# Optimization experiments

Measured on AMD Instinct MI355X. Metric: run time of the kernel, lower is better.

Reference implementation:

```python
import jax, jax.numpy as jnp
import numpy as np

B, T, I, H, O = 64, 1024, 256, 512, 128


def setup_inputs() -> dict:
    key = jax.random.key(0)
    ks = jax.random.split(key, 12)
    s = 1.0 / np.sqrt(H)  # PyTorch LSTM init: U(-1/sqrt(H), 1/sqrt(H))
    u = lambda k, shape: jax.random.uniform(k, shape, jnp.float32, -s, s)
    return {
        "inputs": jax.random.normal(ks[0], (B, T, I), jnp.float32),
        "W_ih_f": u(ks[1], (4 * H, I)),
        "W_hh_f": u(ks[2], (4 * H, H)),
        "b_ih_f": u(ks[3], (4 * H,)),
        "b_hh_f": u(ks[4], (4 * H,)),
        "W_ih_b": u(ks[5], (4 * H, I)),
        "W_hh_b": u(ks[6], (4 * H, H)),
        "b_ih_b": u(ks[7], (4 * H,)),
        "b_hh_b": u(ks[8], (4 * H,)),
        "W_out": u(ks[9], (O, 2 * H)),
        "b_out": u(ks[10], (O,)),
    }


def _lstm_dir(inputs, W_ih, W_hh, b_ih, b_hh, reverse):
    # Precompute input contribution for all timesteps: [B,T,4H] -> [T,B,4H]
    xg = jnp.einsum("bti,gi->btg", inputs, W_ih) + b_ih + b_hh
    xg = jnp.swapaxes(xg, 0, 1)
    b = inputs.shape[0]
    h0 = jnp.zeros((b, H), inputs.dtype)
    c0 = jnp.zeros((b, H), inputs.dtype)

    def step(carry, x_t):
        h, c = carry
        gates = x_t + h @ W_hh.T  # [B,4H], PyTorch gate order i,f,g,o
        i, f, g, o = jnp.split(gates, 4, axis=-1)
        i = jax.nn.sigmoid(i)
        f = jax.nn.sigmoid(f)
        g = jnp.tanh(g)
        o = jax.nn.sigmoid(o)
        c = f * c + i * g
        h = o * jnp.tanh(c)
        return (h, c), h

    (hT, cT), hs = jax.lax.scan(step, (h0, c0), xg, reverse=reverse)
    return jnp.swapaxes(hs, 0, 1), hT, cT  # hs: [B,T,H]


def reference(inputs, W_ih_f, W_hh_f, b_ih_f, b_hh_f,
              W_ih_b, W_hh_b, b_ih_b, b_hh_b, W_out, b_out):
    y_f, h_f, c_f = _lstm_dir(inputs, W_ih_f, W_hh_f, b_ih_f, b_hh_f, False)
    y_b, h_b, c_b = _lstm_dir(inputs, W_ih_b, W_hh_b, b_ih_b, b_hh_b, True)
    y = jnp.concatenate([y_f, y_b], axis=-1)            # [B,T,2H]
    out = jnp.einsum("bth,oh->bto", y, W_out) + b_out    # [B,T,O]
    h_n = jnp.stack([h_f, h_b])                          # [2,B,H]
    c_n = jnp.stack([c_f, c_b])                          # [2,B,H]
    return out, h_n, c_n
```

## Files before the change

kernel.cpp:

```cpp
#include <hip/hip_runtime.h>
#include <stdint.h>

#define T_LEN 1024
#define B_SZ  64
#define I_SZ  256
#define H_SZ  512
#define O_SZ  128
#define WP    776

#define L1_OFF  0ull
#define HB_OFF  524288ull
#define Y_OFF   786432ull
#define XBF_OFF 135004160ull
#define MEMSET_BYTES 786432ull

typedef __attribute__((ext_vector_type(8))) short short8;
typedef __attribute__((ext_vector_type(4))) float f32x4;

__device__ __forceinline__ unsigned short f2bf(float f) {
  unsigned u = __float_as_uint(f);
  u += 0x7fffu + ((u >> 16) & 1u);
  return (unsigned short)(u >> 16);
}
__device__ __forceinline__ ushort4 cvt4(float4 v) {
  ushort4 p;
  p.x = f2bf(v.x); p.y = f2bf(v.y); p.z = f2bf(v.z); p.w = f2bf(v.w);
  return p;
}
__device__ __forceinline__ float sigm(float x) { return 1.0f / (1.0f + __expf(-x)); }
__device__ __forceinline__ float tanh_f(float x) { return 1.0f - 2.0f / (1.0f + __expf(2.0f * x)); }

__global__ void __launch_bounds__(256) cvt_x(const float* __restrict__ x,
                                             unsigned short* __restrict__ xb) {
  size_t i = ((size_t)blockIdx.x * 256 + threadIdx.x) * 8;
  float4 a = *(const float4*)(x + i);
  float4 b = *(const float4*)(x + i + 4);
  *(ushort4*)(xb + i)     = cvt4(a);
  *(ushort4*)(xb + i + 4) = cvt4(b);
}

__global__ void __launch_bounds__(512, 2)
lstm_scan(const unsigned short* __restrict__ xbf,
          const float* __restrict__ WihF, const float* __restrict__ WhhF,
          const float* __restrict__ bihF, const float* __restrict__ bhhF,
          const float* __restrict__ WihB, const float* __restrict__ WhhB,
          const float* __restrict__ bihB, const float* __restrict__ bhhB,
          unsigned char* __restrict__ ws, float* __restrict__ out)
{
  __shared__ unsigned short xh[32 * WP];
  __shared__ float gbuf[4][32][18];
  __shared__ float cst[32][18];

  const int tid  = threadIdx.x;
  const int wave = tid >> 6;
  const int lane = tid & 63;
  const int nl   = lane & 15;
  const int q16  = lane >> 4;

  const int wg  = blockIdx.x;
  const int d   = wg >> 6;
  const int loc = wg & 63;
  const int b0  = (loc >> 5) * 32;
  const int u0  = (loc & 31) * 16;
  const int grp = wg >> 5;

  const float* Wih = d ? WihB : WihF;
  const float* Whh = d ? WhhB : WhhF;
  const float* bih = d ? bihB : bihF;
  const float* bhh = d ? bhhB : bhhF;

  const int gate = wave >> 1;
  const int mt   = wave & 1;

  short8 wfrag[24];
  {
    const int row = gate * H_SZ + u0 + nl;
    const float* wi = Wih + (size_t)row * I_SZ;
    const float* wh = Whh + (size_t)row * H_SZ;
#pragma unroll
    for (int kk = 0; kk < 24; ++kk) {
      const float* src = (kk < 8) ? (wi + kk * 32 + q16 * 8)
                                  : (wh + (kk - 8) * 32 + q16 * 8);
      float4 v0 = ((const float4*)src)[0];
      float4 v1 = ((const float4*)src)[1];
      short8 w;
      w[0] = (short)f2bf(v0.x); w[1] = (short)f2bf(v0.y);
      w[2] = (short)f2bf(v0.z); w[3] = (short)f2bf(v0.w);
      w[4] = (short)f2bf(v1.x); w[5] = (short)f2bf(v1.y);
      w[6] = (short)f2bf(v1.z); w[7] = (short)f2bf(v1.w);
      wfrag[kk] = w;
    }
  }
  const float bias = bih[gate * H_SZ + u0 + nl] + bhh[gate * H_SZ + u0 + nl];

  cst[tid >> 4][tid & 15] = 0.0f;

  unsigned* cntbase = (unsigned*)(ws + L1_OFF);
  unsigned* hbuf32  = (unsigned*)(ws + HB_OFF);
  unsigned* ybuf32  = (unsigned*)(ws + Y_OFF);
  unsigned* xh32    = (unsigned*)xh;

  const int sm = tid >> 4, sseg = tid & 15;

  int t_next = d ? (T_LEN - 1) : 0;
  uint4 px0, px1;
  {
    const uint4* src = (const uint4*)(xbf + ((size_t)(b0 + sm) * T_LEN + t_next) * I_SZ + sseg * 16);
    px0 = src[0]; px1 = src[1];
  }

  for (int s = 0; s < T_LEN; ++s) {
    const int t  = t_next;
    const int rb = (s & 1) ^ 1, wb = s & 1;

    {
      uint4* dst = (uint4*)(xh + sm * WP + sseg * 16);
      dst[0] = px0; dst[1] = px1;
    }
    {
      unsigned hv[16];
#pragma unroll
      for (int j = 0; j < 16; ++j) {
        int lin = j * 512 + tid;
        hv[j] = __hip_atomic_load(hbuf32 + ((size_t)((rb * 2 + d) * B_SZ + b0) * 256 + lin),
                                  __ATOMIC_RELAXED, __HIP_MEMORY_SCOPE_AGENT);
      }
#pragma unroll
      for (int j = 0; j < 16; ++j) {
        int lin = j * 512 + tid;
        int m = lin >> 8, col = lin & 255;
        xh32[m * (WP / 2) + 128 + col] = hv[j];
      }
    }
    __syncthreads();

    f32x4 acc = {0.f, 0.f, 0.f, 0.f};
    const unsigned short* ar = xh + (mt * 16 + nl) * WP + q16 * 8;
#pragma unroll
    for (int kk = 0; kk < 24; ++kk) {
      short8 a = *(const short8*)(ar + kk * 32);
      acc = __builtin_amdgcn_mfma_f32_16x16x32_bf16(a, wfrag[kk], acc, 0, 0, 0);
    }

#pragma unroll
    for (int r = 0; r < 4; ++r) {
      float v = acc[r] + bias;
      v = (gate == 2) ? tanh_f(v) : sigm(v);
      gbuf[gate][mt * 16 + q16 * 4 + r][nl] = v;
    }
    __syncthreads();

    {
      int m = tid >> 4, n = tid & 15;
      float gi = gbuf[0][m][n], gf = gbuf[1][m][n];
      float gg = gbuf[2][m][n], go = gbuf[3][m][n];
      float c = gf * cst[m][n] + gi * gg;
      cst[m][n] = c;
      float h = go * tanh_f(c);
      unsigned hbits = f2bf(h);
      unsigned other = __shfl_xor(hbits, 1);
      if ((tid & 1) == 0) {
        unsigned packed = hbits | (other << 16);
        size_t hi = (size_t)((wb * 2 + d) * B_SZ + b0 + m) * 256 + (u0 + n) / 2;
        __hip_atomic_store(hbuf32 + hi, packed, __ATOMIC_RELAXED, __HIP_MEMORY_SCOPE_AGENT);
        size_t yi = ((size_t)(b0 + m) * T_LEN + t) * 512 + (d * H_SZ + u0 + n) / 2;
        ybuf32[yi] = packed;
      }
      if (s == T_LEN - 1) {
        size_t hi = (size_t)(d * B_SZ + b0 + m) * H_SZ + u0 + n;
        out[8388608ull + hi] = h;
        out[8388608ull + 65536ull + hi] = c;
      }
    }

    if (s < T_LEN - 1) {
      t_next = d ? (T_LEN - 2 - s) : (s + 1);
      {
        const uint4* src = (const uint4*)(xbf + ((size_t)(b0 + sm) * T_LEN + t_next) * I_SZ + sseg * 16);
        px0 = src[0]; px1 = src[1];
      }
      __builtin_amdgcn_s_waitcnt(0);
      __syncthreads();
      if (tid == 0) {
        unsigned* cnt = cntbase + ((size_t)s * 4 + grp) * 32;
        __hip_atomic_fetch_add(cnt, 1u, __ATOMIC_RELAXED, __HIP_MEMORY_SCOPE_AGENT);
        while (__hip_atomic_load(cnt, __ATOMIC_RELAXED, __HIP_MEMORY_SCOPE_AGENT) < 32u)
          __builtin_amdgcn_s_sleep(1);
      }
      __syncthreads();
      __asm__ volatile("" ::: "memory");
    }
  }
}

__global__ void __launch_bounds__(256, 1)
proj(const unsigned short* __restrict__ y, const float* __restrict__ Wout,
     const float* __restrict__ bout, float* __restrict__ out)
{
  __shared__ unsigned short ys[128 * 264];
  __shared__ unsigned short wst[128 * 264];

  const int tid  = threadIdx.x;
  const int wave = tid >> 6;
  const int lane = tid & 63;
  const int nl   = lane & 15;
  const int q16  = lane >> 4;
  const int m0   = blockIdx.x * 128;

  f32x4 acc[2][8];
#pragma unroll
  for (int a = 0; a < 2; ++a)
#pragma unroll
    for (int b = 0; b < 8; ++b) acc[a][b] = (f32x4){0.f, 0.f, 0.f, 0.f};

  for (int k0 = 0; k0 < 1024; k0 += 256) {
    {
      int r = tid >> 1, half = tid & 1;
      const uint4* src = (const uint4*)(y + (size_t)(m0 + r) * 1024 + k0 + half * 128);
      uint4* dst = (uint4*)(ys + r * 264 + half * 128);
#pragma unroll
      for (int q = 0; q < 16; ++q) dst[q] = src[q];
    }
    {
      int r = tid >> 1, half = tid & 1;
      const float4* src = (const float4*)(Wout + (size_t)r * 1024 + k0 + half * 128);
      unsigned short* wd = wst + r * 264 + half * 128;
#pragma unroll
      for (int q = 0; q < 32; ++q) *(ushort4*)(wd + q * 4) = cvt4(src[q]);
    }
    __syncthreads();

#pragma unroll
    for (int kk = 0; kk < 8; ++kk) {
      const int ko = kk * 32 + q16 * 8;
      short8 bfr[8];
#pragma unroll
      for (int nt = 0; nt < 8; ++nt)
        bfr[nt] = *(const short8*)(wst + (nt * 16 + nl) * 264 + ko);
#pragma unroll
      for (int mtt = 0; mtt < 2; ++mtt) {
        short8 a = *(const short8*)(ys + ((wave * 2 + mtt) * 16 + nl) * 264 + ko);
#pragma unroll
        for (int nt = 0; nt < 8; ++nt)
          acc[mtt][nt] = __builtin_amdgcn_mfma_f32_16x16x32_bf16(a, bfr[nt], acc[mtt][nt], 0, 0, 0);
      }
    }
    __syncthreads();
  }

#pragma unroll
  for (int mtt = 0; mtt < 2; ++mtt) {
#pragma unroll
    for (int nt = 0; nt < 8; ++nt) {
      int col = nt * 16 + nl;
      float bo = bout[col];
      int rowb = m0 + (wave * 2 + mtt) * 16 + q16 * 4;
#pragma unroll
      for (int r = 0; r < 4; ++r)
        out[(size_t)(rowb + r) * O_SZ + col] = acc[mtt][nt][r] + bo;
    }
  }
}

extern "C" void kernel_launch(void* const* d_in, const int* in_sizes, int n_in,
                              void* d_out, int out_size, void* d_ws, size_t ws_size,
                              hipStream_t stream) {
  const float* x    = (const float*)d_in[0];
  const float* WihF = (const float*)d_in[1];
  const float* WhhF = (const float*)d_in[2];
  const float* bihF = (const float*)d_in[3];
  const float* bhhF = (const float*)d_in[4];
  const float* WihB = (const float*)d_in[5];
  const float* WhhB = (const float*)d_in[6];
  const float* bihB = (const float*)d_in[7];
  const float* bhhB = (const float*)d_in[8];
  const float* Wout = (const float*)d_in[9];
  const float* bout = (const float*)d_in[10];
  float* out = (float*)d_out;
  unsigned char* ws = (unsigned char*)d_ws;

  hipMemsetAsync(ws, 0, (size_t)MEMSET_BYTES, stream);
  cvt_x<<<8192, 256, 0, stream>>>(x, (unsigned short*)(ws + XBF_OFF));
  lstm_scan<<<128, 512, 0, stream>>>((const unsigned short*)(ws + XBF_OFF),
                                     WihF, WhhF, bihF, bhhF,
                                     WihB, WhhB, bihB, bhhB,
                                     ws, out);
  proj<<<512, 256, 0, stream>>>((const unsigned short*)(ws + Y_OFF), Wout, bout, out);
}
```

Measured before the change: 3.711 ms.

## Replace counter barrier with per-WG step flags and overlap x-projection with sync wait

Swaps the per-step atomic counter barrier (fetch_add plus a single-thread spin and two syncthreads) for per-workgroup monotonic step flags. A whole wave polls the flags and checks them with __all, so there is no atomic RMW and no sleep. The input-projection MFMAs for the next timestep are computed right after the flag is published, before waiting on other workgroups, which takes them off the serial critical path. The recurrent MFMA chain is split into two accumulators to shorten the dependency chain. In exchange, the x tile is double-buffered in LDS and the design depends on relaxed-ordering visibility of the h buffer across workgroups.

```diff
diff --git a/kernel.cpp b/kernel.cpp
--- a/kernel.cpp
+++ b/kernel.cpp
@@ -6,9 +6,8 @@
 #define I_SZ  256
 #define H_SZ  512
 #define O_SZ  128
-#define WP    776
-
-#define L1_OFF  0ull
+
+#define FLAG_OFF 0ull
 #define HB_OFF  524288ull
 #define Y_OFF   786432ull
 #define XBF_OFF 135004160ull
@@ -47,22 +46,24 @@
           const float* __restrict__ bihB, const float* __restrict__ bhhB,
           unsigned char* __restrict__ ws, float* __restrict__ out)
 {
-  __shared__ unsigned short xh[32 * WP];
+  __shared__ unsigned short xs[2][32][264];
+  __shared__ unsigned short hs[32][520];
   __shared__ float gbuf[4][32][18];
   __shared__ float cst[32][18];
 
   const int tid  = threadIdx.x;
+  const int lane = tid & 63;
   const int wave = tid >> 6;
-  const int lane = tid & 63;
   const int nl   = lane & 15;
   const int q16  = lane >> 4;
 
-  const int wg  = blockIdx.x;
-  const int d   = wg >> 6;
-  const int loc = wg & 63;
-  const int b0  = (loc >> 5) * 32;
-  const int u0  = (loc & 31) * 16;
-  const int grp = wg >> 5;
+  const int wg   = blockIdx.x;
+  const int d    = wg >> 6;
+  const int loc  = wg & 63;
+  const int b0   = (loc >> 5) * 32;
+  const int u0   = (loc & 31) * 16;
+  const int grp  = wg >> 5;
+  const int wgid = loc & 31;
 
   const float* Wih = d ? WihB : WihF;
   const float* Whh = d ? WhhB : WhhF;
@@ -95,56 +96,83 @@
 
   cst[tid >> 4][tid & 15] = 0.0f;
 
-  unsigned* cntbase = (unsigned*)(ws + L1_OFF);
-  unsigned* hbuf32  = (unsigned*)(ws + HB_OFF);
-  unsigned* ybuf32  = (unsigned*)(ws + Y_OFF);
-  unsigned* xh32    = (unsigned*)xh;
+  unsigned* flags  = (unsigned*)(ws + FLAG_OFF);
+  unsigned* hbuf32 = (unsigned*)(ws + HB_OFF);
+  unsigned* ybuf32 = (unsigned*)(ws + Y_OFF);
+  unsigned* hs32   = (unsigned*)hs;
 
   const int sm = tid >> 4, sseg = tid & 15;
 
-  int t_next = d ? (T_LEN - 1) : 0;
+  {
+    const int t0 = d ? (T_LEN - 1) : 0;
+    const uint4* src = (const uint4*)(xbf + ((size_t)(b0 + sm) * T_LEN + t0) * I_SZ + sseg * 16);
+    uint4 a = src[0], b = src[1];
+    uint4* dst = (uint4*)(&xs[0][sm][sseg * 16]);
+    dst[0] = a; dst[1] = b;
+  }
+  __syncthreads();
+  f32x4 xacc = {0.f, 0.f, 0.f, 0.f};
+  {
+    const unsigned short* xr = &xs[0][mt * 16 + nl][q16 * 8];
+#pragma unroll
+    for (int kk = 0; kk < 8; ++kk) {
+      short8 a = *(const short8*)(xr + kk * 32);
+      xacc = __builtin_amdgcn_mfma_f32_16x16x32_bf16(a, wfrag[kk], xacc, 0, 0, 0);
+    }
+  }
   uint4 px0, px1;
   {
-    const uint4* src = (const uint4*)(xbf + ((size_t)(b0 + sm) * T_LEN + t_next) * I_SZ + sseg * 16);
+    const int t1 = d ? (T_LEN - 2) : 1;
+    const uint4* src = (const uint4*)(xbf + ((size_t)(b0 + sm) * T_LEN + t1) * I_SZ + sseg * 16);
     px0 = src[0]; px1 = src[1];
   }
 
   for (int s = 0; s < T_LEN; ++s) {
-    const int t  = t_next;
-    const int rb = (s & 1) ^ 1, wb = s & 1;
-
-    {
-      uint4* dst = (uint4*)(xh + sm * WP + sseg * 16);
-      dst[0] = px0; dst[1] = px1;
-    }
+    const int t   = d ? (T_LEN - 1 - s) : s;
+    const int cur = s & 1, nxt = cur ^ 1;
+    const int rb  = cur ^ 1, wb = cur;
+
+    if (s > 0) {
+      const unsigned tgt = (unsigned)s;
+      unsigned* fl = flags + grp * 32;
+      for (;;) {
+        unsigned f = (lane < 32)
+          ? __hip_atomic_load(fl + lane, __ATOMIC_RELAXED, __HIP_MEMORY_SCOPE_AGENT)
+          : tgt;
+        if (__all((int)(f >= tgt))) break;
+      }
+    }
+
     {
       unsigned hv[16];
+      unsigned* hb = hbuf32 + (size_t)((rb * 2 + d) * B_SZ + b0) * 256;
+#pragma unroll
+      for (int j = 0; j < 16; ++j)
+        hv[j] = __hip_atomic_load(hb + j * 512 + tid, __ATOMIC_RELAXED, __HIP_MEMORY_SCOPE_AGENT);
 #pragma unroll
       for (int j = 0; j < 16; ++j) {
         int lin = j * 512 + tid;
-        hv[j] = __hip_atomic_load(hbuf32 + ((size_t)((rb * 2 + d) * B_SZ + b0) * 256 + lin),
-                                  __ATOMIC_RELAXED, __HIP_MEMORY_SCOPE_AGENT);
-      }
-#pragma unroll
-      for (int j = 0; j < 16; ++j) {
-        int lin = j * 512 + tid;
-        int m = lin >> 8, col = lin & 255;
-        xh32[m * (WP / 2) + 128 + col] = hv[j];
-      }
-    }
-    __syncthreads();
-
-    f32x4 acc = {0.f, 0.f, 0.f, 0.f};
-    const unsigned short* ar = xh + (mt * 16 + nl) * WP + q16 * 8;
-#pragma unroll
-    for (int kk = 0; kk < 24; ++kk) {
-      short8 a = *(const short8*)(ar + kk * 32);
-      acc = __builtin_amdgcn_mfma_f32_16x16x32_bf16(a, wfrag[kk], acc, 0, 0, 0);
+        hs32[(lin >> 8) * 260 + (lin & 255)] = hv[j];
+      }
+    }
+    __syncthreads();
+
+    f32x4 acc0 = xacc, acc1 = {0.f, 0.f, 0.f, 0.f};
+    {
+      const unsigned short* ar = &hs[mt * 16 + nl][q16 * 8];
+#pragma unroll
+      for (int kk = 0; kk < 16; kk += 2) {
+        short8 a0 = *(const short8*)(ar + kk * 32);
+        short8 a1 = *(const short8*)(ar + (kk + 1) * 32);
+        acc0 = __builtin_amdgcn_mfma_f32_16x16x32_bf16(a0, wfrag[8 + kk], acc0, 0, 0, 0);
+        acc1 = __builtin_amdgcn_mfma_f32_16x16x32_bf16(a1, wfrag[9 + kk], acc1, 0, 0, 0);
+      }
+      acc0 += acc1;
     }
 
 #pragma unroll
     for (int r = 0; r < 4; ++r) {
-      float v = acc[r] + bias;
+      float v = acc0[r] + bias;
       v = (gate == 2) ? tanh_f(v) : sigm(v);
       gbuf[gate][mt * 16 + q16 * 4 + r][nl] = v;
     }
@@ -174,21 +202,29 @@
     }
 
     if (s < T_LEN - 1) {
-      t_next = d ? (T_LEN - 2 - s) : (s + 1);
-      {
-        const uint4* src = (const uint4*)(xbf + ((size_t)(b0 + sm) * T_LEN + t_next) * I_SZ + sseg * 16);
+      uint4* dst = (uint4*)(&xs[nxt][sm][sseg * 16]);
+      dst[0] = px0; dst[1] = px1;
+    }
+    __builtin_amdgcn_s_waitcnt(0);
+    __syncthreads();
+
+    if (s < T_LEN - 1) {
+      if (tid == 0)
+        __hip_atomic_store(flags + grp * 32 + wgid, (unsigned)(s + 1),
+                           __ATOMIC_RELAXED, __HIP_MEMORY_SCOPE_AGENT);
+      if (s + 2 < T_LEN) {
+        const int t2 = d ? (T_LEN - 3 - s) : (s + 2);
+        const uint4* src = (const uint4*)(xbf + ((size_t)(b0 + sm) * T_LEN + t2) * I_SZ + sseg * 16);
         px0 = src[0]; px1 = src[1];
       }
-      __builtin_amdgcn_s_waitcnt(0);
-      __syncthreads();
-      if (tid == 0) {
-        unsigned* cnt = cntbase + ((size_t)s * 4 + grp) * 32;
-        __hip_atomic_fetch_add(cnt, 1u, __ATOMIC_RELAXED, __HIP_MEMORY_SCOPE_AGENT);
-        while (__hip_atomic_load(cnt, __ATOMIC_RELAXED, __HIP_MEMORY_SCOPE_AGENT) < 32u)
-          __builtin_amdgcn_s_sleep(1);
-      }
-      __syncthreads();
-      __asm__ volatile("" ::: "memory");
+      f32x4 xa = {0.f, 0.f, 0.f, 0.f};
+      const unsigned short* xr = &xs[nxt][mt * 16 + nl][q16 * 8];
+#pragma unroll
+      for (int kk = 0; kk < 8; ++kk) {
+        short8 a = *(const short8*)(xr + kk * 32);
+        xa = __builtin_amdgcn_mfma_f32_16x16x32_bf16(a, wfrag[kk], xa, 0, 0, 0);
+      }
+      xacc = xa;
     }
   }
 }
```

After: 3.375 ms. -9.0%, faster.
